# Kernel optimization log

Hardware: AMD Instinct MI355X
Metric: run time of the kernel (lower is better)

## Reference

```python
import jax, jax.numpy as jnp
import numpy as np

N_NODES = 100000
N_EDGES = 3200000
IN_DIM = 256
OUT_DIM = 256


def setup_inputs() -> dict:
    key = jax.random.key(0)
    k1, k2, k3, k4, k5 = jax.random.split(key, 5)
    x = jax.random.normal(k1, (N_NODES, IN_DIM), dtype=jnp.float32)
    edge_src = jax.random.randint(k2, (N_EDGES,), 0, N_NODES, dtype=jnp.int32)
    edge_dst = jax.random.randint(k3, (N_EDGES,), 0, N_NODES, dtype=jnp.int32)
    # normalized adjacency values (e.g. D^-1/2 A D^-1/2 entries)
    edge_val = jax.random.uniform(k4, (N_EDGES,), dtype=jnp.float32)
    # parameters: uniform(0,1) weight, constant 0.3 bias (matches torch init)
    weight = jax.random.uniform(k5, (IN_DIM, OUT_DIM), dtype=jnp.float32)
    bias = jnp.full((OUT_DIM,), 0.3, dtype=jnp.float32)
    return {"x": x, "edge_src": edge_src, "edge_dst": edge_dst,
            "edge_val": edge_val, "weight": weight, "bias": bias}


def reference(x, edge_src, edge_dst, edge_val, weight, bias):
    # dense feature transform: [N, in] @ [in, out] -> [N, out]
    h = x @ weight
    # sparse adjacency aggregation: out[d] = sum_e val[e] * h[src[e]] for dst[e]==d
    msgs = edge_val[:, None] * h[edge_src]              # [E, out]
    agg = jax.ops.segment_sum(msgs, edge_dst, num_segments=N_NODES)
    return agg + bias
```

## Files before the change

kernel.cpp:

```cpp
#include <hip/hip_runtime.h>

#define FDIM 256
#define BSH 6
#define NBMAX 1600
#define CH 4096
#define NSLOT 7
#define CAPB 2432
#define EPT 10

typedef __attribute__((ext_vector_type(4))) float f32x4;
typedef __attribute__((ext_vector_type(8))) short bf16x8;
typedef unsigned long long u64;

static __device__ __forceinline__ unsigned short f32_to_bf16_rtn(float f) {
    unsigned u = __builtin_bit_cast(unsigned, f);
    u += 0x7FFFu + ((u >> 16) & 1u);
    return (unsigned short)(u >> 16);
}
static __device__ __forceinline__ float bf16_to_f32(unsigned short s) {
    unsigned u = ((unsigned)s) << 16;
    return __builtin_bit_cast(float, u);
}

__global__ __launch_bounds__(256) void bin_kernel(
    const int* __restrict__ src, const int* __restrict__ dst, const float* __restrict__ val,
    int* __restrict__ cursors, u64* __restrict__ binned, int n_edges, int nb,
    const float* __restrict__ W, unsigned short* __restrict__ wfrag) {
    __shared__ int hist[NBMAX];
    __shared__ int gbase[NBMAX];
    __shared__ int sbase[NBMAX];
    __shared__ int scan_s[256];
    __shared__ u64 stage[CH];
    __shared__ unsigned short bos[CH];

    const int t = threadIdx.x;

    if (blockIdx.x < 32) {
        int tt = blockIdx.x * 256 + t;
        int lane = tt & 63;
        int kt   = (tt >> 6) & 7;
        int nt   = tt >> 9;
        int col  = nt * 16 + (lane & 15);
        int k0   = kt * 32 + 8 * (lane >> 4);
        ushort4 o0, o1;
        o0.x = f32_to_bf16_rtn(W[(k0 + 0) * FDIM + col]);
        o0.y = f32_to_bf16_rtn(W[(k0 + 1) * FDIM + col]);
        o0.z = f32_to_bf16_rtn(W[(k0 + 2) * FDIM + col]);
        o0.w = f32_to_bf16_rtn(W[(k0 + 3) * FDIM + col]);
        o1.x = f32_to_bf16_rtn(W[(k0 + 4) * FDIM + col]);
        o1.y = f32_to_bf16_rtn(W[(k0 + 5) * FDIM + col]);
        o1.z = f32_to_bf16_rtn(W[(k0 + 6) * FDIM + col]);
        o1.w = f32_to_bf16_rtn(W[(k0 + 7) * FDIM + col]);
        ((ushort4*)(wfrag + (size_t)tt * 8))[0] = o0;
        ((ushort4*)(wfrag + (size_t)tt * 8))[1] = o1;
    }

    const int chunk0 = blockIdx.x * CH;
    const int m = min(CH, n_edges - chunk0);
    if (m <= 0) return;

    for (int b = t; b < nb; b += 256) hist[b] = 0;
    __syncthreads();
    for (int i = t; i < m; i += 256) atomicAdd(&hist[dst[chunk0 + i] >> BSH], 1);
    __syncthreads();
    for (int b = t; b < nb; b += 256) {
        int c = hist[b];
        gbase[b] = c ? atomicAdd(&cursors[b], c) : 0;
    }
    int loc[NSLOT]; int sum = 0;
    #pragma unroll
    for (int k = 0; k < NSLOT; ++k) {
        int b = t * NSLOT + k;
        int c = (b < nb) ? hist[b] : 0;
        loc[k] = sum; sum += c;
    }
    scan_s[t] = sum;
    __syncthreads();
    #pragma unroll
    for (int off = 1; off < 256; off <<= 1) {
        int u = (t >= off) ? scan_s[t - off] : 0;
        __syncthreads();
        scan_s[t] += u;
        __syncthreads();
    }
    int excl = scan_s[t] - sum;
    #pragma unroll
    for (int k = 0; k < NSLOT; ++k) {
        int b = t * NSLOT + k;
        if (b < nb) sbase[b] = excl + loc[k];
    }
    __syncthreads();
    for (int b = t; b < nb; b += 256) hist[b] = 0;
    __syncthreads();
    for (int i = t; i < m; i += 256) {
        int d = dst[chunk0 + i];
        int b = d >> BSH;
        int p = atomicAdd(&hist[b], 1);
        int slot = sbase[b] + p;
        unsigned w0 = (unsigned)src[chunk0 + i] | ((unsigned)(d & 63) << 17);
        unsigned w1 = __builtin_bit_cast(unsigned, val[chunk0 + i]);
        stage[slot] = (u64)w0 | ((u64)w1 << 32);
        bos[slot]   = (unsigned short)b;
    }
    __syncthreads();
    for (int i = t; i < m; i += 256) {
        int b = bos[i];
        int p = gbase[b] + (i - sbase[b]);
        if (p < CAPB)
            binned[(size_t)b * CAPB + p] = stage[i];
    }
}

__global__ __launch_bounds__(256) void gemm_h_kernel(
    const float* __restrict__ x, const unsigned short* __restrict__ wfrag,
    unsigned short* __restrict__ hb, int n_rows) {
    int wave = (int)((blockIdx.x * 256u + threadIdx.x) >> 6);
    int lane = threadIdx.x & 63;
    int m0 = wave * 32;
    if (m0 >= n_rows) return;

    f32x4 acc[2][16];
    #pragma unroll
    for (int s = 0; s < 2; ++s)
        #pragma unroll
        for (int i = 0; i < 16; ++i) acc[s][i] = (f32x4)(0.f);

    const int arow0 = m0 + (lane & 15);
    const int arow1 = arow0 + 16;
    const int kbase = 8 * (lane >> 4);

    #pragma unroll
    for (int kt = 0; kt < 8; ++kt) {
        const f32x4* ap0 = (const f32x4*)(x + (size_t)arow0 * FDIM + kt * 32 + kbase);
        const f32x4* ap1 = (const f32x4*)(x + (size_t)arow1 * FDIM + kt * 32 + kbase);
        f32x4 a0 = __builtin_nontemporal_load(ap0);
        f32x4 a1 = __builtin_nontemporal_load(ap0 + 1);
        f32x4 b0 = __builtin_nontemporal_load(ap1);
        f32x4 b1 = __builtin_nontemporal_load(ap1 + 1);
        bf16x8 af0, af1;
        #pragma unroll
        for (int j = 0; j < 4; ++j) {
            af0[j]     = (short)f32_to_bf16_rtn(a0[j]);
            af0[j + 4] = (short)f32_to_bf16_rtn(a1[j]);
            af1[j]     = (short)f32_to_bf16_rtn(b0[j]);
            af1[j + 4] = (short)f32_to_bf16_rtn(b1[j]);
        }
        #pragma unroll
        for (int nt = 0; nt < 16; ++nt) {
            bf16x8 bfr = *(const bf16x8*)(wfrag + ((size_t)(nt * 8 + kt) * 64 + lane) * 8);
            acc[0][nt] = __builtin_amdgcn_mfma_f32_16x16x32_bf16(af0, bfr, acc[0][nt], 0, 0, 0);
            acc[1][nt] = __builtin_amdgcn_mfma_f32_16x16x32_bf16(af1, bfr, acc[1][nt], 0, 0, 0);
        }
    }

    const int col = lane & 15;
    #pragma unroll
    for (int s = 0; s < 2; ++s) {
        const int rbase = m0 + s * 16 + 4 * (lane >> 4);
        #pragma unroll
        for (int nt = 0; nt < 16; ++nt) {
            #pragma unroll
            for (int r = 0; r < 4; ++r) {
                int row = rbase + r;
                if (row < n_rows)
                    __builtin_nontemporal_store(f32_to_bf16_rtn(acc[s][nt][r]),
                        &hb[(size_t)row * FDIM + nt * 16 + col]);
            }
        }
    }
}

__global__ __launch_bounds__(256) void gather_kernel(
    const unsigned short* __restrict__ hb, const int* __restrict__ cursors,
    const u64* __restrict__ binned, const float* __restrict__ bias,
    float* __restrict__ out, int n_nodes) {
    __shared__ u64 s2[CAPB];
    __shared__ int cnt[64], startv[64], cur[64];

    const int t = threadIdx.x, b = blockIdx.x;
    const size_t base = (size_t)b * CAPB;
    int m = cursors[b];
    if (m > CAPB) m = CAPB;

    if (t < 64) cnt[t] = 0;
    __syncthreads();
    u64 ereg[EPT];
    int nmine = 0;
    #pragma unroll
    for (int k = 0; k < EPT; ++k) {
        int i = t + k * 256;
        if (i < m) {
            u64 e = binned[base + i];
            ereg[k] = e;
            nmine = k + 1;
            atomicAdd(&cnt[(int)((e >> 17) & 63)], 1);
        }
    }
    __syncthreads();
    if (t < 64) startv[t] = cnt[t];
    __syncthreads();
    #pragma unroll
    for (int off = 1; off < 64; off <<= 1) {
        int u = 0;
        if (t < 64 && t >= off) u = startv[t - off];
        __syncthreads();
        if (t < 64) startv[t] += u;
        __syncthreads();
    }
    if (t < 64) cur[t] = startv[t] - cnt[t];
    __syncthreads();
    #pragma unroll
    for (int k = 0; k < EPT; ++k) {
        if (k < nmine) {
            u64 e = ereg[k];
            int p = atomicAdd(&cur[(int)((e >> 17) & 63)], 1);
            s2[p] = e;
        }
    }
    __syncthreads();

    const int wv = t >> 6, lane = t & 63;
    const int half = lane >> 5, l32 = lane & 31;
    const int dbase = (l32 << 3) + (half << 2);
    const f32x4 bv = *(const f32x4*)(bias + dbase);

    for (int q = 0; q < 16; ++q) {
        const int lo = wv * 16 + q;
        const int node = (b << BSH) + lo;
        const int beg = startv[lo] - cnt[lo];
        const int end = startv[lo];
        float acc[8] = {0.f, 0.f, 0.f, 0.f, 0.f, 0.f, 0.f, 0.f};
        int j = beg;
        for (; j + 16 <= end; j += 16) {
            #pragma unroll
            for (int k = 0; k < 8; ++k) {
                u64 e = s2[j + 2 * k + half];
                float v = __builtin_bit_cast(float, (unsigned)(e >> 32));
                bf16x8 r = *(const bf16x8*)(hb + (((size_t)((unsigned)e & 0x1FFFF)) << 8) + (l32 << 3));
                #pragma unroll
                for (int d = 0; d < 8; ++d)
                    acc[d] += v * bf16_to_f32((unsigned short)r[d]);
            }
        }
        for (; j + 8 <= end; j += 8) {
            #pragma unroll
            for (int k = 0; k < 4; ++k) {
                u64 e = s2[j + 2 * k + half];
                float v = __builtin_bit_cast(float, (unsigned)(e >> 32));
                bf16x8 r = *(const bf16x8*)(hb + (((size_t)((unsigned)e & 0x1FFFF)) << 8) + (l32 << 3));
                #pragma unroll
                for (int d = 0; d < 8; ++d)
                    acc[d] += v * bf16_to_f32((unsigned short)r[d]);
            }
        }
        for (; j < end; j += 2) {
            int idx = j + half;
            u64 e = s2[idx < end ? idx : j];
            float v = (idx < end) ? __builtin_bit_cast(float, (unsigned)(e >> 32)) : 0.f;
            bf16x8 r = *(const bf16x8*)(hb + (((size_t)((unsigned)e & 0x1FFFF)) << 8) + (l32 << 3));
            #pragma unroll
            for (int d = 0; d < 8; ++d)
                acc[d] += v * bf16_to_f32((unsigned short)r[d]);
        }
        #pragma unroll
        for (int d = 0; d < 8; ++d) acc[d] += __shfl_xor(acc[d], 32);
        if (node < n_nodes) {
            f32x4 o = {acc[4 * half + 0] + bv[0], acc[4 * half + 1] + bv[1],
                       acc[4 * half + 2] + bv[2], acc[4 * half + 3] + bv[3]};
            __builtin_nontemporal_store(o, (f32x4*)(out + ((size_t)node << 8) + dbase));
        }
    }
}

extern "C" void kernel_launch(void* const* d_in, const int* in_sizes, int n_in,
                              void* d_out, int out_size, void* d_ws, size_t ws_size,
                              hipStream_t stream) {
    const float* x    = (const float*)d_in[0];
    const int*   src  = (const int*)  d_in[1];
    const int*   dst  = (const int*)  d_in[2];
    const float* val  = (const float*)d_in[3];
    const float* W    = (const float*)d_in[4];
    const float* bias = (const float*)d_in[5];
    float* out = (float*)d_out;

    int n_nodes = in_sizes[0] / FDIM;
    int n_edges = in_sizes[1];
    int nb = (n_nodes + 63) >> BSH;

    int* cursors = (int*)d_ws;
    size_t ioff = ((size_t)nb + 1) & ~(size_t)1;
    u64* binned = (u64*)((int*)d_ws + ioff);
    unsigned short* hb    = (unsigned short*)(binned + (size_t)nb * CAPB);
    unsigned short* wfrag = hb + (size_t)n_nodes * FDIM;

    (void)hipMemsetAsync(cursors, 0, (size_t)nb * sizeof(int), stream);

    int bin_blocks = (n_edges + CH - 1) / CH;
    bin_kernel<<<bin_blocks, 256, 0, stream>>>(src, dst, val, cursors, binned, n_edges, nb,
                                               W, wfrag);

    int waves = (n_nodes + 31) / 32;
    int gemm_blocks = (waves + 3) / 4;
    gemm_h_kernel<<<gemm_blocks, 256, 0, stream>>>(x, wfrag, hb, n_nodes);

    gather_kernel<<<nb, 256, 0, stream>>>(hb, cursors, binned, bias, out, n_nodes);
}
```

Measured before the change: 493.4 us.

## Co-schedule edge binning with the GEMM in one interleaved kernel, widen bins to 128 nodes

Edge binning and the dense GEMM now run as a single launch: even blocks bin edges and odd blocks compute bf16 h tiles, so the two independent stages overlap on the GPU. The weight conversion and cursor zeroing move into a small setup kernel, which replaces the memset. Buckets grow from 64 to 128 destination nodes, which halves the gather block count and doubles per-bucket capacity and per-thread edge registers. The larger bins raise LDS and register pressure in both the bin and gather kernels, and may lower occupancy.

```diff
diff --git a/kernel.cpp b/kernel.cpp
--- a/kernel.cpp
+++ b/kernel.cpp
@@ -1,12 +1,12 @@
 #include <hip/hip_runtime.h>
 
 #define FDIM 256
-#define BSH 6
-#define NBMAX 1600
+#define BSH 7
+#define NBMAX 800
 #define CH 4096
-#define NSLOT 7
-#define CAPB 2432
-#define EPT 10
+#define NSLOT 4
+#define CAPB 4864
+#define EPT 19
 
 typedef __attribute__((ext_vector_type(4))) float f32x4;
 typedef __attribute__((ext_vector_type(8))) short bf16x8;
@@ -22,10 +22,38 @@
     return __builtin_bit_cast(float, u);
 }
 
-__global__ __launch_bounds__(256) void bin_kernel(
+__global__ __launch_bounds__(256) void setup_kernel(const float* __restrict__ W,
+                                                    unsigned short* __restrict__ wfrag,
+                                                    int* __restrict__ cursors, int nb) {
+    const int t = threadIdx.x;
+    if (blockIdx.x == 32) {
+        for (int i = t; i < nb; i += 256) cursors[i] = 0;
+        return;
+    }
+    int tt = blockIdx.x * 256 + t;
+    int lane = tt & 63;
+    int kt   = (tt >> 6) & 7;
+    int nt   = tt >> 9;
+    int col  = nt * 16 + (lane & 15);
+    int k0   = kt * 32 + 8 * (lane >> 4);
+    ushort4 o0, o1;
+    o0.x = f32_to_bf16_rtn(W[(k0 + 0) * FDIM + col]);
+    o0.y = f32_to_bf16_rtn(W[(k0 + 1) * FDIM + col]);
+    o0.z = f32_to_bf16_rtn(W[(k0 + 2) * FDIM + col]);
+    o0.w = f32_to_bf16_rtn(W[(k0 + 3) * FDIM + col]);
+    o1.x = f32_to_bf16_rtn(W[(k0 + 4) * FDIM + col]);
+    o1.y = f32_to_bf16_rtn(W[(k0 + 5) * FDIM + col]);
+    o1.z = f32_to_bf16_rtn(W[(k0 + 6) * FDIM + col]);
+    o1.w = f32_to_bf16_rtn(W[(k0 + 7) * FDIM + col]);
+    ((ushort4*)(wfrag + (size_t)tt * 8))[0] = o0;
+    ((ushort4*)(wfrag + (size_t)tt * 8))[1] = o1;
+}
+
+__global__ __launch_bounds__(256) void bin_gemm_kernel(
     const int* __restrict__ src, const int* __restrict__ dst, const float* __restrict__ val,
-    int* __restrict__ cursors, u64* __restrict__ binned, int n_edges, int nb,
-    const float* __restrict__ W, unsigned short* __restrict__ wfrag) {
+    int* __restrict__ cursors, u64* __restrict__ binned, int n_edges, int nb, int bin_blocks,
+    const float* __restrict__ x, const unsigned short* __restrict__ wfrag,
+    unsigned short* __restrict__ hb, int n_rows) {
     __shared__ int hist[NBMAX];
     __shared__ int gbase[NBMAX];
     __shared__ int sbase[NBMAX];
@@ -34,30 +62,68 @@
     __shared__ unsigned short bos[CH];
 
     const int t = threadIdx.x;
-
-    if (blockIdx.x < 32) {
-        int tt = blockIdx.x * 256 + t;
-        int lane = tt & 63;
-        int kt   = (tt >> 6) & 7;
-        int nt   = tt >> 9;
-        int col  = nt * 16 + (lane & 15);
-        int k0   = kt * 32 + 8 * (lane >> 4);
-        ushort4 o0, o1;
-        o0.x = f32_to_bf16_rtn(W[(k0 + 0) * FDIM + col]);
-        o0.y = f32_to_bf16_rtn(W[(k0 + 1) * FDIM + col]);
-        o0.z = f32_to_bf16_rtn(W[(k0 + 2) * FDIM + col]);
-        o0.w = f32_to_bf16_rtn(W[(k0 + 3) * FDIM + col]);
-        o1.x = f32_to_bf16_rtn(W[(k0 + 4) * FDIM + col]);
-        o1.y = f32_to_bf16_rtn(W[(k0 + 5) * FDIM + col]);
-        o1.z = f32_to_bf16_rtn(W[(k0 + 6) * FDIM + col]);
-        o1.w = f32_to_bf16_rtn(W[(k0 + 7) * FDIM + col]);
-        ((ushort4*)(wfrag + (size_t)tt * 8))[0] = o0;
-        ((ushort4*)(wfrag + (size_t)tt * 8))[1] = o1;
-    }
-
-    const int chunk0 = blockIdx.x * CH;
+    const int sub = blockIdx.x >> 1;
+
+    if (blockIdx.x & 1) {
+        const int wv = t >> 6, lane = t & 63;
+        const int m0 = sub * 128 + wv * 32;
+        if (m0 >= n_rows) return;
+
+        f32x4 acc[2][16];
+        #pragma unroll
+        for (int s = 0; s < 2; ++s)
+            #pragma unroll
+            for (int i = 0; i < 16; ++i) acc[s][i] = (f32x4)(0.f);
+
+        const int arow0 = m0 + (lane & 15);
+        const int arow1 = arow0 + 16;
+        const int kbase = 8 * (lane >> 4);
+
+        #pragma unroll
+        for (int kt = 0; kt < 8; ++kt) {
+            const f32x4* ap0 = (const f32x4*)(x + (size_t)arow0 * FDIM + kt * 32 + kbase);
+            const f32x4* ap1 = (const f32x4*)(x + (size_t)arow1 * FDIM + kt * 32 + kbase);
+            f32x4 a0 = __builtin_nontemporal_load(ap0);
+            f32x4 a1 = __builtin_nontemporal_load(ap0 + 1);
+            f32x4 b0 = __builtin_nontemporal_load(ap1);
+            f32x4 b1 = __builtin_nontemporal_load(ap1 + 1);
+            bf16x8 af0, af1;
+            #pragma unroll
+            for (int j = 0; j < 4; ++j) {
+                af0[j]     = (short)f32_to_bf16_rtn(a0[j]);
+                af0[j + 4] = (short)f32_to_bf16_rtn(a1[j]);
+                af1[j]     = (short)f32_to_bf16_rtn(b0[j]);
+                af1[j + 4] = (short)f32_to_bf16_rtn(b1[j]);
+            }
+            #pragma unroll
+            for (int nt = 0; nt < 16; ++nt) {
+                bf16x8 bfr = *(const bf16x8*)(wfrag + ((size_t)(nt * 8 + kt) * 64 + lane) * 8);
+                acc[0][nt] = __builtin_amdgcn_mfma_f32_16x16x32_bf16(af0, bfr, acc[0][nt], 0, 0, 0);
+                acc[1][nt] = __builtin_amdgcn_mfma_f32_16x16x32_bf16(af1, bfr, acc[1][nt], 0, 0, 0);
+            }
+        }
+
+        const int col = lane & 15;
+        #pragma unroll
+        for (int s = 0; s < 2; ++s) {
+            const int rbase = m0 + s * 16 + 4 * (lane >> 4);
+            #pragma unroll
+            for (int nt = 0; nt < 16; ++nt) {
+                #pragma unroll
+                for (int r = 0; r < 4; ++r) {
+                    int row = rbase + r;
+                    if (row < n_rows)
+                        __builtin_nontemporal_store(f32_to_bf16_rtn(acc[s][nt][r]),
+                            &hb[(size_t)row * FDIM + nt * 16 + col]);
+                }
+            }
+        }
+        return;
+    }
+
+    if (sub >= bin_blocks) return;
+    const int chunk0 = sub * CH;
     const int m = min(CH, n_edges - chunk0);
-    if (m <= 0) return;
 
     for (int b = t; b < nb; b += 256) hist[b] = 0;
     __syncthreads();
@@ -97,7 +163,7 @@
         int b = d >> BSH;
         int p = atomicAdd(&hist[b], 1);
         int slot = sbase[b] + p;
-        unsigned w0 = (unsigned)src[chunk0 + i] | ((unsigned)(d & 63) << 17);
+        unsigned w0 = (unsigned)src[chunk0 + i] | ((unsigned)(d & 127) << 17);
         unsigned w1 = __builtin_bit_cast(unsigned, val[chunk0 + i]);
         stage[slot] = (u64)w0 | ((u64)w1 << 32);
         bos[slot]   = (unsigned short)b;
@@ -111,78 +177,19 @@
     }
 }
 
-__global__ __launch_bounds__(256) void gemm_h_kernel(
-    const float* __restrict__ x, const unsigned short* __restrict__ wfrag,
-    unsigned short* __restrict__ hb, int n_rows) {
-    int wave = (int)((blockIdx.x * 256u + threadIdx.x) >> 6);
-    int lane = threadIdx.x & 63;
-    int m0 = wave * 32;
-    if (m0 >= n_rows) return;
-
-    f32x4 acc[2][16];
-    #pragma unroll
-    for (int s = 0; s < 2; ++s)
-        #pragma unroll
-        for (int i = 0; i < 16; ++i) acc[s][i] = (f32x4)(0.f);
-
-    const int arow0 = m0 + (lane & 15);
-    const int arow1 = arow0 + 16;
-    const int kbase = 8 * (lane >> 4);
-
-    #pragma unroll
-    for (int kt = 0; kt < 8; ++kt) {
-        const f32x4* ap0 = (const f32x4*)(x + (size_t)arow0 * FDIM + kt * 32 + kbase);
-        const f32x4* ap1 = (const f32x4*)(x + (size_t)arow1 * FDIM + kt * 32 + kbase);
-        f32x4 a0 = __builtin_nontemporal_load(ap0);
-        f32x4 a1 = __builtin_nontemporal_load(ap0 + 1);
-        f32x4 b0 = __builtin_nontemporal_load(ap1);
-        f32x4 b1 = __builtin_nontemporal_load(ap1 + 1);
-        bf16x8 af0, af1;
-        #pragma unroll
-        for (int j = 0; j < 4; ++j) {
-            af0[j]     = (short)f32_to_bf16_rtn(a0[j]);
-            af0[j + 4] = (short)f32_to_bf16_rtn(a1[j]);
-            af1[j]     = (short)f32_to_bf16_rtn(b0[j]);
-            af1[j + 4] = (short)f32_to_bf16_rtn(b1[j]);
-        }
-        #pragma unroll
-        for (int nt = 0; nt < 16; ++nt) {
-            bf16x8 bfr = *(const bf16x8*)(wfrag + ((size_t)(nt * 8 + kt) * 64 + lane) * 8);
-            acc[0][nt] = __builtin_amdgcn_mfma_f32_16x16x32_bf16(af0, bfr, acc[0][nt], 0, 0, 0);
-            acc[1][nt] = __builtin_amdgcn_mfma_f32_16x16x32_bf16(af1, bfr, acc[1][nt], 0, 0, 0);
-        }
-    }
-
-    const int col = lane & 15;
-    #pragma unroll
-    for (int s = 0; s < 2; ++s) {
-        const int rbase = m0 + s * 16 + 4 * (lane >> 4);
-        #pragma unroll
-        for (int nt = 0; nt < 16; ++nt) {
-            #pragma unroll
-            for (int r = 0; r < 4; ++r) {
-                int row = rbase + r;
-                if (row < n_rows)
-                    __builtin_nontemporal_store(f32_to_bf16_rtn(acc[s][nt][r]),
-                        &hb[(size_t)row * FDIM + nt * 16 + col]);
-            }
-        }
-    }
-}
-
 __global__ __launch_bounds__(256) void gather_kernel(
     const unsigned short* __restrict__ hb, const int* __restrict__ cursors,
     const u64* __restrict__ binned, const float* __restrict__ bias,
     float* __restrict__ out, int n_nodes) {
     __shared__ u64 s2[CAPB];
-    __shared__ int cnt[64], startv[64], cur[64];
+    __shared__ int cnt[128], startv[128], cur[128];
 
     const int t = threadIdx.x, b = blockIdx.x;
     const size_t base = (size_t)b * CAPB;
     int m = cursors[b];
     if (m > CAPB) m = CAPB;
 
-    if (t < 64) cnt[t] = 0;
+    if (t < 128) cnt[t] = 0;
     __syncthreads();
     u64 ereg[EPT];
     int nmine = 0;
@@ -193,27 +200,27 @@
             u64 e = binned[base + i];
             ereg[k] = e;
             nmine = k + 1;
-            atomicAdd(&cnt[(int)((e >> 17) & 63)], 1);
-        }
-    }
-    __syncthreads();
-    if (t < 64) startv[t] = cnt[t];
-    __syncthreads();
-    #pragma unroll
-    for (int off = 1; off < 64; off <<= 1) {
+            atomicAdd(&cnt[(int)((e >> 17) & 127)], 1);
+        }
+    }
+    __syncthreads();
+    if (t < 128) startv[t] = cnt[t];
+    __syncthreads();
+    #pragma unroll
+    for (int off = 1; off < 128; off <<= 1) {
         int u = 0;
-        if (t < 64 && t >= off) u = startv[t - off];
+        if (t < 128 && t >= off) u = startv[t - off];
         __syncthreads();
-        if (t < 64) startv[t] += u;
+        if (t < 128) startv[t] += u;
         __syncthreads();
     }
-    if (t < 64) cur[t] = startv[t] - cnt[t];
+    if (t < 128) cur[t] = startv[t] - cnt[t];
     __syncthreads();
     #pragma unroll
     for (int k = 0; k < EPT; ++k) {
         if (k < nmine) {
             u64 e = ereg[k];
-            int p = atomicAdd(&cur[(int)((e >> 17) & 63)], 1);
+            int p = atomicAdd(&cur[(int)((e >> 17) & 127)], 1);
             s2[p] = e;
         }
     }
@@ -224,8 +231,8 @@
     const int dbase = (l32 << 3) + (half << 2);
     const f32x4 bv = *(const f32x4*)(bias + dbase);
 
-    for (int q = 0; q < 16; ++q) {
-        const int lo = wv * 16 + q;
+    for (int q = 0; q < 32; ++q) {
+        const int lo = wv * 32 + q;
         const int node = (b << BSH) + lo;
         const int beg = startv[lo] - cnt[lo];
         const int end = startv[lo];
@@ -285,7 +292,7 @@
 
     int n_nodes = in_sizes[0] / FDIM;
     int n_edges = in_sizes[1];
-    int nb = (n_nodes + 63) >> BSH;
+    int nb = (n_nodes + 127) >> BSH;
 
     int* cursors = (int*)d_ws;
     size_t ioff = ((size_t)nb + 1) & ~(size_t)1;
@@ -293,15 +300,14 @@
     unsigned short* hb    = (unsigned short*)(binned + (size_t)nb * CAPB);
     unsigned short* wfrag = hb + (size_t)n_nodes * FDIM;
 
-    (void)hipMemsetAsync(cursors, 0, (size_t)nb * sizeof(int), stream);
-
-    int bin_blocks = (n_edges + CH - 1) / CH;
-    bin_kernel<<<bin_blocks, 256, 0, stream>>>(src, dst, val, cursors, binned, n_edges, nb,
-                                               W, wfrag);
-
-    int waves = (n_nodes + 31) / 32;
-    int gemm_blocks = (waves + 3) / 4;
-    gemm_h_kernel<<<gemm_blocks, 256, 0, stream>>>(x, wfrag, hb, n_nodes);
+    setup_kernel<<<33, 256, 0, stream>>>(W, wfrag, cursors, nb);
+
+    int bin_blocks  = (n_edges + CH - 1) / CH;
+    int gemm_blocks = (n_nodes + 127) / 128;
+    int npairs = max(bin_blocks, gemm_blocks);
+    bin_gemm_kernel<<<npairs * 2, 256, 0, stream>>>(src, dst, val, cursors, binned,
+                                                    n_edges, nb, bin_blocks,
+                                                    x, wfrag, hb, n_nodes);
 
     gather_kernel<<<nb, 256, 0, stream>>>(hb, cursors, binned, bias, out, n_nodes);
 }
```

After: 503.0 us. Within noise of the previous version (+1.9%).

## Split W conversion into setup kernel, drop bos array, reorder bin after GEMM

Applied to the files above, without the earlier changes.

Moves the weight bf16 conversion and the cursor zeroing into a small setup kernel, which replaces the memset launch. The bin kernel now packs the full destination index into the 64-bit edge word, truncating the value's two low mantissa bits, so the separate shared bin-index array is no longer needed. That shrinks shared memory and may raise occupancy. The bin kernel now runs after the GEMM, which changes cache residency for the edge data before the gather, at a small cost in value precision.

```diff
diff --git a/kernel.cpp b/kernel.cpp
--- a/kernel.cpp
+++ b/kernel.cpp
@@ -22,93 +22,31 @@
     return __builtin_bit_cast(float, u);
 }
 
-__global__ __launch_bounds__(256) void bin_kernel(
-    const int* __restrict__ src, const int* __restrict__ dst, const float* __restrict__ val,
-    int* __restrict__ cursors, u64* __restrict__ binned, int n_edges, int nb,
-    const float* __restrict__ W, unsigned short* __restrict__ wfrag) {
-    __shared__ int hist[NBMAX];
-    __shared__ int gbase[NBMAX];
-    __shared__ int sbase[NBMAX];
-    __shared__ int scan_s[256];
-    __shared__ u64 stage[CH];
-    __shared__ unsigned short bos[CH];
-
+__global__ __launch_bounds__(256) void setup_kernel(const float* __restrict__ W,
+                                                    unsigned short* __restrict__ wfrag,
+                                                    int* __restrict__ cursors, int nb) {
     const int t = threadIdx.x;
-
-    if (blockIdx.x < 32) {
-        int tt = blockIdx.x * 256 + t;
-        int lane = tt & 63;
-        int kt   = (tt >> 6) & 7;
-        int nt   = tt >> 9;
-        int col  = nt * 16 + (lane & 15);
-        int k0   = kt * 32 + 8 * (lane >> 4);
-        ushort4 o0, o1;
-        o0.x = f32_to_bf16_rtn(W[(k0 + 0) * FDIM + col]);
-        o0.y = f32_to_bf16_rtn(W[(k0 + 1) * FDIM + col]);
-        o0.z = f32_to_bf16_rtn(W[(k0 + 2) * FDIM + col]);
-        o0.w = f32_to_bf16_rtn(W[(k0 + 3) * FDIM + col]);
-        o1.x = f32_to_bf16_rtn(W[(k0 + 4) * FDIM + col]);
-        o1.y = f32_to_bf16_rtn(W[(k0 + 5) * FDIM + col]);
-        o1.z = f32_to_bf16_rtn(W[(k0 + 6) * FDIM + col]);
-        o1.w = f32_to_bf16_rtn(W[(k0 + 7) * FDIM + col]);
-        ((ushort4*)(wfrag + (size_t)tt * 8))[0] = o0;
-        ((ushort4*)(wfrag + (size_t)tt * 8))[1] = o1;
-    }
-
-    const int chunk0 = blockIdx.x * CH;
-    const int m = min(CH, n_edges - chunk0);
-    if (m <= 0) return;
-
-    for (int b = t; b < nb; b += 256) hist[b] = 0;
-    __syncthreads();
-    for (int i = t; i < m; i += 256) atomicAdd(&hist[dst[chunk0 + i] >> BSH], 1);
-    __syncthreads();
-    for (int b = t; b < nb; b += 256) {
-        int c = hist[b];
-        gbase[b] = c ? atomicAdd(&cursors[b], c) : 0;
-    }
-    int loc[NSLOT]; int sum = 0;
-    #pragma unroll
-    for (int k = 0; k < NSLOT; ++k) {
-        int b = t * NSLOT + k;
-        int c = (b < nb) ? hist[b] : 0;
-        loc[k] = sum; sum += c;
-    }
-    scan_s[t] = sum;
-    __syncthreads();
-    #pragma unroll
-    for (int off = 1; off < 256; off <<= 1) {
-        int u = (t >= off) ? scan_s[t - off] : 0;
-        __syncthreads();
-        scan_s[t] += u;
-        __syncthreads();
-    }
-    int excl = scan_s[t] - sum;
-    #pragma unroll
-    for (int k = 0; k < NSLOT; ++k) {
-        int b = t * NSLOT + k;
-        if (b < nb) sbase[b] = excl + loc[k];
-    }
-    __syncthreads();
-    for (int b = t; b < nb; b += 256) hist[b] = 0;
-    __syncthreads();
-    for (int i = t; i < m; i += 256) {
-        int d = dst[chunk0 + i];
-        int b = d >> BSH;
-        int p = atomicAdd(&hist[b], 1);
-        int slot = sbase[b] + p;
-        unsigned w0 = (unsigned)src[chunk0 + i] | ((unsigned)(d & 63) << 17);
-        unsigned w1 = __builtin_bit_cast(unsigned, val[chunk0 + i]);
-        stage[slot] = (u64)w0 | ((u64)w1 << 32);
-        bos[slot]   = (unsigned short)b;
-    }
-    __syncthreads();
-    for (int i = t; i < m; i += 256) {
-        int b = bos[i];
-        int p = gbase[b] + (i - sbase[b]);
-        if (p < CAPB)
-            binned[(size_t)b * CAPB + p] = stage[i];
-    }
+    if (blockIdx.x == 32) {
+        for (int i = t; i < nb; i += 256) cursors[i] = 0;
+        return;
+    }
+    int tt = blockIdx.x * 256 + t;
+    int lane = tt & 63;
+    int kt   = (tt >> 6) & 7;
+    int nt   = tt >> 9;
+    int col  = nt * 16 + (lane & 15);
+    int k0   = kt * 32 + 8 * (lane >> 4);
+    ushort4 o0, o1;
+    o0.x = f32_to_bf16_rtn(W[(k0 + 0) * FDIM + col]);
+    o0.y = f32_to_bf16_rtn(W[(k0 + 1) * FDIM + col]);
+    o0.z = f32_to_bf16_rtn(W[(k0 + 2) * FDIM + col]);
+    o0.w = f32_to_bf16_rtn(W[(k0 + 3) * FDIM + col]);
+    o1.x = f32_to_bf16_rtn(W[(k0 + 4) * FDIM + col]);
+    o1.y = f32_to_bf16_rtn(W[(k0 + 5) * FDIM + col]);
+    o1.z = f32_to_bf16_rtn(W[(k0 + 6) * FDIM + col]);
+    o1.w = f32_to_bf16_rtn(W[(k0 + 7) * FDIM + col]);
+    ((ushort4*)(wfrag + (size_t)tt * 8))[0] = o0;
+    ((ushort4*)(wfrag + (size_t)tt * 8))[1] = o1;
 }
 
 __global__ __launch_bounds__(256) void gemm_h_kernel(
@@ -167,6 +105,71 @@
                         &hb[(size_t)row * FDIM + nt * 16 + col]);
             }
         }
+    }
+}
+
+__global__ __launch_bounds__(256) void bin_kernel(
+    const int* __restrict__ src, const int* __restrict__ dst, const float* __restrict__ val,
+    int* __restrict__ cursors, u64* __restrict__ binned, int n_edges, int nb) {
+    __shared__ int hist[NBMAX];
+    __shared__ int gbase[NBMAX];
+    __shared__ int sbase[NBMAX];
+    __shared__ int scan_s[256];
+    __shared__ u64 stage[CH];
+
+    const int t = threadIdx.x;
+    const int chunk0 = blockIdx.x * CH;
+    const int m = min(CH, n_edges - chunk0);
+    if (m <= 0) return;
+
+    for (int b = t; b < nb; b += 256) hist[b] = 0;
+    __syncthreads();
+    for (int i = t; i < m; i += 256) atomicAdd(&hist[dst[chunk0 + i] >> BSH], 1);
+    __syncthreads();
+    for (int b = t; b < nb; b += 256) {
+        int c = hist[b];
+        gbase[b] = c ? atomicAdd(&cursors[b], c) : 0;
+    }
+    int loc[NSLOT]; int sum = 0;
+    #pragma unroll
+    for (int k = 0; k < NSLOT; ++k) {
+        int b = t * NSLOT + k;
+        int c = (b < nb) ? hist[b] : 0;
+        loc[k] = sum; sum += c;
+    }
+    scan_s[t] = sum;
+    __syncthreads();
+    #pragma unroll
+    for (int off = 1; off < 256; off <<= 1) {
+        int u = (t >= off) ? scan_s[t - off] : 0;
+        __syncthreads();
+        scan_s[t] += u;
+        __syncthreads();
+    }
+    int excl = scan_s[t] - sum;
+    #pragma unroll
+    for (int k = 0; k < NSLOT; ++k) {
+        int b = t * NSLOT + k;
+        if (b < nb) sbase[b] = excl + loc[k];
+    }
+    __syncthreads();
+    for (int b = t; b < nb; b += 256) hist[b] = 0;
+    __syncthreads();
+    for (int i = t; i < m; i += 256) {
+        int d = dst[chunk0 + i];
+        int b = d >> BSH;
+        int p = atomicAdd(&hist[b], 1);
+        unsigned vb = __builtin_bit_cast(unsigned, val[chunk0 + i]);
+        stage[sbase[b] + p] = (u64)(unsigned)src[chunk0 + i]
+                            | ((u64)(unsigned)d << 17) | ((u64)(vb >> 2) << 34);
+    }
+    __syncthreads();
+    for (int i = t; i < m; i += 256) {
+        u64 e = stage[i];
+        int b = (int)((e >> 17) & 0x1FFFF) >> BSH;
+        int p = gbase[b] + (i - sbase[b]);
+        if (p < CAPB)
+            binned[(size_t)b * CAPB + p] = e;
     }
 }
 
@@ -235,7 +238,7 @@
             #pragma unroll
             for (int k = 0; k < 8; ++k) {
                 u64 e = s2[j + 2 * k + half];
-                float v = __builtin_bit_cast(float, (unsigned)(e >> 32));
+                float v = __builtin_bit_cast(float, ((unsigned)(e >> 34)) << 2);
                 bf16x8 r = *(const bf16x8*)(hb + (((size_t)((unsigned)e & 0x1FFFF)) << 8) + (l32 << 3));
                 #pragma unroll
                 for (int d = 0; d < 8; ++d)
@@ -246,7 +249,7 @@
             #pragma unroll
             for (int k = 0; k < 4; ++k) {
                 u64 e = s2[j + 2 * k + half];
-                float v = __builtin_bit_cast(float, (unsigned)(e >> 32));
+                float v = __builtin_bit_cast(float, ((unsigned)(e >> 34)) << 2);
                 bf16x8 r = *(const bf16x8*)(hb + (((size_t)((unsigned)e & 0x1FFFF)) << 8) + (l32 << 3));
                 #pragma unroll
                 for (int d = 0; d < 8; ++d)
@@ -256,7 +259,7 @@
         for (; j < end; j += 2) {
             int idx = j + half;
             u64 e = s2[idx < end ? idx : j];
-            float v = (idx < end) ? __builtin_bit_cast(float, (unsigned)(e >> 32)) : 0.f;
+            float v = (idx < end) ? __builtin_bit_cast(float, ((unsigned)(e >> 34)) << 2) : 0.f;
             bf16x8 r = *(const bf16x8*)(hb + (((size_t)((unsigned)e & 0x1FFFF)) << 8) + (l32 << 3));
             #pragma unroll
             for (int d = 0; d < 8; ++d)
@@ -293,15 +296,14 @@
     unsigned short* hb    = (unsigned short*)(binned + (size_t)nb * CAPB);
     unsigned short* wfrag = hb + (size_t)n_nodes * FDIM;
 
-    (void)hipMemsetAsync(cursors, 0, (size_t)nb * sizeof(int), stream);
-
-    int bin_blocks = (n_edges + CH - 1) / CH;
-    bin_kernel<<<bin_blocks, 256, 0, stream>>>(src, dst, val, cursors, binned, n_edges, nb,
-                                               W, wfrag);
+    setup_kernel<<<33, 256, 0, stream>>>(W, wfrag, cursors, nb);
 
     int waves = (n_nodes + 31) / 32;
     int gemm_blocks = (waves + 3) / 4;
     gemm_h_kernel<<<gemm_blocks, 256, 0, stream>>>(x, wfrag, hb, n_nodes);
 
+    int bin_blocks = (n_edges + CH - 1) / CH;
+    bin_kernel<<<bin_blocks, 256, 0, stream>>>(src, dst, val, cursors, binned, n_edges, nb);
+
     gather_kernel<<<nb, 256, 0, stream>>>(hb, cursors, binned, bias, out, n_nodes);
 }
```

New measurement: 497.4 us. No clear change (+0.8%).
